# Performance work log

Measured on AMD Instinct MI355X. Metric: run time of the kernel, lower is better.

The kernel has to match this reference:

```python
import jax, jax.numpy as jnp
import numpy as np

T, H, N = 4096, 2048, 1024  # seq_length, d_model, d_hidden
MAX_PHASE = 6.28


def setup_inputs() -> dict:
    key = jax.random.key(0)
    ks = jax.random.split(key, 9)
    inputs = jax.random.normal(ks[0], (T, H), dtype=jnp.float32)
    # LRU init (exp_param=True, r_min=0, r_max=1): lambda = exp(-exp(nu) + i*exp(theta))
    u1 = jax.random.uniform(ks[1], (N,), dtype=jnp.float32)
    u2 = jax.random.uniform(ks[2], (N,), dtype=jnp.float32)
    nu = jnp.log(-0.5 * jnp.log(u1))            # log-parameterized decay
    theta = jnp.log(MAX_PHASE * u2)             # log-parameterized phase
    # gamma_log = log(sqrt(1 - |lambda|^2)), |lambda| = exp(-exp(nu))
    gamma_log = 0.5 * jnp.log(1.0 - jnp.exp(-2.0 * jnp.exp(nu)) + 1e-8)
    B_re = jax.random.normal(ks[3], (N, H), dtype=jnp.float32) / np.sqrt(2 * H)
    B_im = jax.random.normal(ks[4], (N, H), dtype=jnp.float32) / np.sqrt(2 * H)
    C_re = jax.random.normal(ks[5], (H, N), dtype=jnp.float32) / np.sqrt(N)
    C_im = jax.random.normal(ks[6], (H, N), dtype=jnp.float32) / np.sqrt(N)
    D = jax.random.normal(ks[7], (H,), dtype=jnp.float32)
    return {"inputs": inputs, "nu": nu, "theta": theta, "gamma_log": gamma_log,
            "B_re": B_re, "B_im": B_im, "C_re": C_re, "C_im": C_im, "D": D}


def _binary_operator_diag(q_i, q_j):
    A_i, b_i = q_i
    A_j, b_j = q_j
    return (A_j * A_i, A_j * b_i + b_j)


def reference(inputs, nu, theta, gamma_log, B_re, B_im, C_re, C_im, D):
    # diag_lambda = exp(-exp(nu) + i*exp(theta))   (exp_param=True)
    diag_lambda = jnp.exp(-jnp.exp(nu) + 1j * jnp.exp(theta))      # [N] complex64
    gamma = jnp.exp(gamma_log)                                      # [N]
    B_norm = (B_re + 1j * B_im) * gamma[:, None]                    # [N, H] complex
    # Bu_t = B_norm @ u_t  ->  [T, N]
    Bu = inputs.astype(jnp.complex64) @ B_norm.T
    Lam = jnp.broadcast_to(diag_lambda[None, :], Bu.shape)          # [T, N]
    # parallel scan of diagonal linear recurrence h_t = lambda * h_{t-1} + Bu_t
    _, h = jax.lax.associative_scan(_binary_operator_diag, (Lam, Bu))
    C = C_re + 1j * C_im                                            # [H, N]
    # y_t = Re(C @ h_t) + D * u_t
    y = (h @ C.T).real + D[None, :] * inputs                        # [T, H]
    return y
```

## Files before the change

### kernel.cpp

```cpp
#include <hip/hip_runtime.h>
#include <math.h>

#define T_DIM 4096
#define H_DIM 2048
#define N_DIM 1024
#define N2    2048
#define KK    2048
#define CHUNK 64
#define NCHUNK (T_DIM / CHUNK)
#define NT    (KK / 64)

using u16    = unsigned short;
using u16x4  = __attribute__((ext_vector_type(4))) u16;
using bf16x8 = __attribute__((ext_vector_type(8))) short;
using f32x4  = __attribute__((ext_vector_type(4))) float;

typedef const __attribute__((address_space(1))) u16 glob_u16;
typedef __attribute__((address_space(3))) u16 lds_u16;

__device__ inline void gload16(const u16* g, u16* l) {
    __builtin_amdgcn_global_load_lds((glob_u16*)g, (lds_u16*)l, 16, 0, 0);
}

__device__ inline u16 f2bf(float x) {
    unsigned u = __builtin_bit_cast(unsigned, x);
    u += 0x7fffu + ((u >> 16) & 1u);
    return (u16)(u >> 16);
}
__device__ inline float bf2f(u16 x) {
    return __builtin_bit_cast(float, (unsigned)x << 16);
}

__global__ __launch_bounds__(256) void cvt_u_k(const float* __restrict__ X,
                                               u16* __restrict__ Y) {
    size_t i = ((size_t)blockIdx.x * 256 + threadIdx.x) * 4;
    float4 v = *(const float4*)(X + i);
    u16x4 o = { f2bf(v.x), f2bf(v.y), f2bf(v.z), f2bf(v.w) };
    *(u16x4*)(Y + i) = o;
}

__global__ __launch_bounds__(256) void cvt_b_k(const float* __restrict__ Bre,
                                               const float* __restrict__ Bim,
                                               const float* __restrict__ glog,
                                               u16* __restrict__ Bcat) {
    size_t i = ((size_t)blockIdx.x * 256 + threadIdx.x) * 4;
    int n = (int)(i >> 11);
    size_t h = i & 2047;
    int nn = n & (N_DIM - 1);
    float g = expf(glog[nn]);
    const float* src = (n < N_DIM ? Bre : Bim) + (size_t)nn * H_DIM + h;
    float4 v = *(const float4*)src;
    u16x4 o = { f2bf(v.x * g), f2bf(v.y * g), f2bf(v.z * g), f2bf(v.w * g) };
    *(u16x4*)(Bcat + i) = o;
}

__global__ __launch_bounds__(256) void cvt_c_k(const float* __restrict__ Cre,
                                               const float* __restrict__ Cim,
                                               u16* __restrict__ Ccat) {
    size_t i = ((size_t)blockIdx.x * 256 + threadIdx.x) * 4;
    int hrow = (int)(i >> 11);
    int n = (int)(i & 2047);
    float sgn = 1.f;
    const float* src;
    if (n < N_DIM) src = Cre + (size_t)hrow * N_DIM + n;
    else { src = Cim + (size_t)hrow * N_DIM + (n - N_DIM); sgn = -1.f; }
    float4 v = *(const float4*)src;
    u16x4 o = { f2bf(v.x * sgn), f2bf(v.y * sgn), f2bf(v.z * sgn), f2bf(v.w * sgn) };
    *(u16x4*)(Ccat + i) = o;
}

template <int EPI>
__global__ __launch_bounds__(512, 2) void gemm_pipe(
    const u16* __restrict__ A, const u16* __restrict__ B,
    float* __restrict__ C, const float* __restrict__ D,
    const u16* __restrict__ Ubf)
{
    __shared__ u16 lds[65536];

    const int tid  = threadIdx.x;
    const int wave = tid >> 6, lane = tid & 63;
    const int nbid = (blockIdx.x & 7) * 32 + (blockIdx.x >> 3);
    const int bm = nbid >> 4;
    const int bn = nbid & 15;
    const size_t row0 = (size_t)bm * 256;
    const size_t col0 = (size_t)bn * 128;
    const int wr = wave >> 1, wc = wave & 1;
    const int fr = lane & 15, fq = lane >> 4;

    const int srow = tid >> 3;
    const int skc  = (tid & 7) ^ (srow & 7);
    const u16* aSrc = A + (row0 + srow) * KK + skc * 8;
    const u16* bSrc = B + (col0 + srow) * KK + skc * 8;

    const int aBase = (wr * 64 + fr) * 64;
    const int bBase = (wc * 64 + fr) * 64;
    const int swzk[2] = { ((fq) ^ (fr & 7)) * 8, ((4 + fq) ^ (fr & 7)) * 8 };

    f32x4 acc[4][4] = {};

    auto STAGE_A = [&](int buf, int kt) {
#pragma unroll
        for (int u = 0; u < 4; ++u)
            gload16(aSrc + (size_t)u * 64 * KK + kt * 64,
                    &lds[buf * 16384 + u * 4096 + wave * 512]);
    };
    auto STAGE_B = [&](int buf, int kt) {
#pragma unroll
        for (int u = 0; u < 2; ++u)
            gload16(bSrc + (size_t)u * 64 * KK + kt * 64,
                    &lds[49152 + buf * 8192 + u * 4096 + wave * 512]);
    };

    STAGE_A(0, 0); STAGE_B(0, 0); STAGE_A(1, 1);
    asm volatile("s_waitcnt vmcnt(4)\n\ts_barrier" ::: "memory");

    int a_cur = 0;
#pragma unroll 2
    for (int t = 0; t < NT; ++t) {
        const u16* Ab = &lds[a_cur * 16384];
        const u16* Bb = &lds[49152 + (t & 1) * 8192];
        bf16x8 af[4], bfv[4];

#pragma unroll
        for (int m = 0; m < 4; ++m)
            af[m] = *(const bf16x8*)&Ab[aBase + m * 1024 + swzk[0]];
#pragma unroll
        for (int n = 0; n < 4; ++n)
            bfv[n] = *(const bf16x8*)&Bb[bBase + n * 1024 + swzk[0]];
        if (t + 1 < NT) STAGE_B((t + 1) & 1, t + 1);
        asm volatile("s_barrier\n\ts_waitcnt lgkmcnt(0)" ::: "memory");
        __builtin_amdgcn_s_setprio(1);
#pragma unroll
        for (int m = 0; m < 4; ++m)
#pragma unroll
            for (int n = 0; n < 4; ++n)
                acc[m][n] = __builtin_amdgcn_mfma_f32_16x16x32_bf16(
                    af[m], bfv[n], acc[m][n], 0, 0, 0);
        __builtin_amdgcn_s_setprio(0);
        asm volatile("s_barrier" ::: "memory");

#pragma unroll
        for (int m = 0; m < 4; ++m)
            af[m] = *(const bf16x8*)&Ab[aBase + m * 1024 + swzk[1]];
#pragma unroll
        for (int n = 0; n < 4; ++n)
            bfv[n] = *(const bf16x8*)&Bb[bBase + n * 1024 + swzk[1]];
        if (t + 2 < NT) {
            int a_nxt = a_cur - 1; if (a_nxt < 0) a_nxt = 2;
            STAGE_A(a_nxt, t + 2);
        }
        if (t + 2 < NT)
            asm volatile("s_waitcnt vmcnt(4)\n\ts_barrier\n\ts_waitcnt lgkmcnt(0)" ::: "memory");
        else if (t + 1 < NT)
            asm volatile("s_waitcnt vmcnt(0)\n\ts_barrier\n\ts_waitcnt lgkmcnt(0)" ::: "memory");
        else
            asm volatile("s_barrier\n\ts_waitcnt lgkmcnt(0)" ::: "memory");
        __builtin_amdgcn_s_setprio(1);
#pragma unroll
        for (int m = 0; m < 4; ++m)
#pragma unroll
            for (int n = 0; n < 4; ++n)
                acc[m][n] = __builtin_amdgcn_mfma_f32_16x16x32_bf16(
                    af[m], bfv[n], acc[m][n], 0, 0, 0);
        __builtin_amdgcn_s_setprio(0);
        asm volatile("s_barrier" ::: "memory");

        ++a_cur; if (a_cur == 3) a_cur = 0;
    }

    const int crow = (int)row0 + wr * 64 + fq * 4;
    const int ccol = (int)col0 + wc * 64 + fr;
    float dc[4];
    if constexpr (EPI) {
#pragma unroll
        for (int n = 0; n < 4; ++n) dc[n] = D[ccol + n * 16];
    }
#pragma unroll
    for (int m = 0; m < 4; ++m)
#pragma unroll
        for (int n = 0; n < 4; ++n) {
            int cc = ccol + n * 16;
#pragma unroll
            for (int j = 0; j < 4; ++j) {
                int r = crow + m * 16 + j;
                size_t p = (size_t)r * N2 + cc;
                float v = acc[m][n][j];
                if constexpr (EPI) v += dc[n] * bf2f(Ubf[p]);
                C[p] = v;
            }
        }
}

__global__ __launch_bounds__(256) void carry_pass_k(const float* __restrict__ Bu,
                                                    const float* __restrict__ nu,
                                                    const float* __restrict__ theta,
                                                    float* __restrict__ car) {
    int idx = blockIdx.x * 256 + threadIdx.x;
    int chan = idx & (N_DIM - 1);
    int chunk = idx >> 10;
    float a = expf(nu[chan]), b = expf(theta[chan]);
    float m = expf(-a), s, c;
    __sincosf(b, &s, &c);
    float lr = m * c, li = m * s;
    float hr = 0.f, hi = 0.f;
    size_t base = (size_t)chunk * CHUNK * N2 + chan;
    for (int i = 0; i < CHUNK; ++i) {
        size_t p = base + (size_t)i * N2;
        float br = Bu[p], bi = Bu[p + N_DIM];
        float nr = fmaf(lr, hr, fmaf(-li, hi, br));
        float ni = fmaf(lr, hi, fmaf(li, hr, bi));
        hr = nr; hi = ni;
    }
    car[(size_t)chunk * N2 + chan] = hr;
    car[(size_t)chunk * N2 + N_DIM + chan] = hi;
}

__global__ __launch_bounds__(256) void scan_carry_k(float* __restrict__ car,
                                                    const float* __restrict__ nu,
                                                    const float* __restrict__ theta) {
    __shared__ float sR[NCHUNK][65], sI[NCHUNK][65];
    int tid = threadIdx.x;
    int chan0 = blockIdx.x * 64;
    for (int i = tid; i < NCHUNK * 64; i += 256) {
        int ck = i >> 6, c = i & 63;
        sR[ck][c] = car[(size_t)ck * N2 + chan0 + c];
        sI[ck][c] = car[(size_t)ck * N2 + N_DIM + chan0 + c];
    }
    __syncthreads();
    if (tid < 64) {
        int chan = chan0 + tid;
        float a = expf(nu[chan]), b = expf(theta[chan]);
        float m = expf(-(float)CHUNK * a), s, c;
        __sincosf((float)CHUNK * b, &s, &c);
        float lr = m * c, li = m * s;
        float hr = sR[0][tid], hi = sI[0][tid];
        for (int ck = 1; ck < NCHUNK; ++ck) {
            float nr = fmaf(lr, hr, fmaf(-li, hi, sR[ck][tid]));
            float ni = fmaf(lr, hi, fmaf(li, hr, sI[ck][tid]));
            hr = nr; hi = ni;
            sR[ck][tid] = hr; sI[ck][tid] = hi;
        }
    }
    __syncthreads();
    for (int i = tid; i < NCHUNK * 64; i += 256) {
        int ck = i >> 6, c = i & 63;
        car[(size_t)ck * N2 + chan0 + c] = sR[ck][c];
        car[(size_t)ck * N2 + N_DIM + chan0 + c] = sI[ck][c];
    }
}

__global__ __launch_bounds__(256) void scan_out_k(const float* __restrict__ Bu,
                                                  const float* __restrict__ car,
                                                  const float* __restrict__ nu,
                                                  const float* __restrict__ theta,
                                                  u16* __restrict__ Hbf) {
    int idx = blockIdx.x * 256 + threadIdx.x;
    int chan = idx & (N_DIM - 1);
    int chunk = idx >> 10;
    float a = expf(nu[chan]), b = expf(theta[chan]);
    float m = expf(-a), s, c;
    __sincosf(b, &s, &c);
    float lr = m * c, li = m * s;
    float hr = 0.f, hi = 0.f;
    if (chunk > 0) {
        size_t cp = (size_t)(chunk - 1) * N2 + chan;
        hr = car[cp]; hi = car[cp + N_DIM];
    }
    size_t base = (size_t)chunk * CHUNK * N2 + chan;
    for (int i = 0; i < CHUNK; ++i) {
        size_t p = base + (size_t)i * N2;
        float br = Bu[p], bi = Bu[p + N_DIM];
        float nr = fmaf(lr, hr, fmaf(-li, hi, br));
        float ni = fmaf(lr, hi, fmaf(li, hr, bi));
        hr = nr; hi = ni;
        Hbf[p] = f2bf(hr);
        Hbf[p + N_DIM] = f2bf(hi);
    }
}

extern "C" void kernel_launch(void* const* d_in, const int* in_sizes, int n_in,
                              void* d_out, int out_size, void* d_ws, size_t ws_size,
                              hipStream_t stream) {
    const float* U     = (const float*)d_in[0];
    const float* nu    = (const float*)d_in[1];
    const float* theta = (const float*)d_in[2];
    const float* glog  = (const float*)d_in[3];
    const float* Bre   = (const float*)d_in[4];
    const float* Bim   = (const float*)d_in[5];
    const float* Cre   = (const float*)d_in[6];
    const float* Cim   = (const float*)d_in[7];
    const float* Dp    = (const float*)d_in[8];
    float* Y = (float*)d_out;

    u16* Ubf  = (u16*)d_ws;
    u16* Bcat = Ubf + (size_t)T_DIM * H_DIM;
    u16* Ccat = Bcat + (size_t)N2 * H_DIM;
    u16* Hbf  = Ccat + (size_t)H_DIM * N2;
    float* Bu = (float*)(Hbf + (size_t)T_DIM * N2);
    float* car = Bu + (size_t)T_DIM * N2;

    cvt_u_k<<<(T_DIM * H_DIM / 4) / 256, 256, 0, stream>>>(U, Ubf);
    cvt_b_k<<<((size_t)N2 * H_DIM / 4) / 256, 256, 0, stream>>>(Bre, Bim, glog, Bcat);
    cvt_c_k<<<((size_t)H_DIM * N2 / 4) / 256, 256, 0, stream>>>(Cre, Cim, Ccat);

    gemm_pipe<0><<<256, 512, 0, stream>>>(Ubf, Bcat, Bu, nullptr, nullptr);

    carry_pass_k<<<(NCHUNK * N_DIM) / 256, 256, 0, stream>>>(Bu, nu, theta, car);
    scan_carry_k<<<N_DIM / 64, 256, 0, stream>>>(car, nu, theta);
    scan_out_k<<<(NCHUNK * N_DIM) / 256, 256, 0, stream>>>(Bu, car, nu, theta, Hbf);

    gemm_pipe<1><<<256, 512, 0, stream>>>(Hbf, Ccat, Y, Dp, Ubf);
}
```

Baseline: 121.7 us.

## Software-pipeline LDS fragment reads across iterations and cut per-iteration barriers

The GEMM main loop now keeps two sets of register fragments. The first-half fragments of the next K tile are read from LDS right after a single barrier at the end of each iteration, while the second-half reads sit between the two MFMA groups. This drops the loop from four barriers per iteration to one and lets LDS reads overlap MFMA work. Launch bounds move from 2 to 1 blocks per CU, giving the compiler room for the extra fragment registers. The risk is higher register pressure and less latency hiding from the compiler's own scheduling, since the unroll pragma was also removed.

```diff
diff --git a/kernel.cpp b/kernel.cpp
--- a/kernel.cpp
+++ b/kernel.cpp
@@ -70,7 +70,7 @@
 }
 
 template <int EPI>
-__global__ __launch_bounds__(512, 2) void gemm_pipe(
+__global__ __launch_bounds__(512, 1) void gemm_pipe(
     const u16* __restrict__ A, const u16* __restrict__ B,
     float* __restrict__ C, const float* __restrict__ D,
     const u16* __restrict__ Ubf)
@@ -94,7 +94,8 @@
 
     const int aBase = (wr * 64 + fr) * 64;
     const int bBase = (wc * 64 + fr) * 64;
-    const int swzk[2] = { ((fq) ^ (fr & 7)) * 8, ((4 + fq) ^ (fr & 7)) * 8 };
+    const int swz0 = ((fq)     ^ (fr & 7)) * 8;
+    const int swz1 = ((4 + fq) ^ (fr & 7)) * 8;
 
     f32x4 acc[4][4] = {};
 
@@ -111,60 +112,67 @@
                     &lds[49152 + buf * 8192 + u * 4096 + wave * 512]);
     };
 
+    bf16x8 fa[4], fb[4], ga[4], gb[4];
+
+    auto READ_F = [&](const u16* Ab, const u16* Bb, int swz) {
+#pragma unroll
+        for (int m = 0; m < 4; ++m) fa[m] = *(const bf16x8*)&Ab[aBase + m * 1024 + swz];
+#pragma unroll
+        for (int n = 0; n < 4; ++n) fb[n] = *(const bf16x8*)&Bb[bBase + n * 1024 + swz];
+    };
+    auto READ_G = [&](const u16* Ab, const u16* Bb, int swz) {
+#pragma unroll
+        for (int m = 0; m < 4; ++m) ga[m] = *(const bf16x8*)&Ab[aBase + m * 1024 + swz];
+#pragma unroll
+        for (int n = 0; n < 4; ++n) gb[n] = *(const bf16x8*)&Bb[bBase + n * 1024 + swz];
+    };
+    auto MFMA_F = [&]() {
+        __builtin_amdgcn_s_setprio(1);
+#pragma unroll
+        for (int m = 0; m < 4; ++m)
+#pragma unroll
+            for (int n = 0; n < 4; ++n)
+                acc[m][n] = __builtin_amdgcn_mfma_f32_16x16x32_bf16(
+                    fa[m], fb[n], acc[m][n], 0, 0, 0);
+        __builtin_amdgcn_s_setprio(0);
+    };
+    auto MFMA_G = [&]() {
+        __builtin_amdgcn_s_setprio(1);
+#pragma unroll
+        for (int m = 0; m < 4; ++m)
+#pragma unroll
+            for (int n = 0; n < 4; ++n)
+                acc[m][n] = __builtin_amdgcn_mfma_f32_16x16x32_bf16(
+                    ga[m], gb[n], acc[m][n], 0, 0, 0);
+        __builtin_amdgcn_s_setprio(0);
+    };
+
     STAGE_A(0, 0); STAGE_B(0, 0); STAGE_A(1, 1);
-    asm volatile("s_waitcnt vmcnt(4)\n\ts_barrier" ::: "memory");
+    asm volatile("s_waitcnt vmcnt(4)" ::: "memory");
+    __builtin_amdgcn_s_barrier();
+    READ_F(&lds[0], &lds[49152], swz0);
 
     int a_cur = 0;
-#pragma unroll 2
     for (int t = 0; t < NT; ++t) {
         const u16* Ab = &lds[a_cur * 16384];
         const u16* Bb = &lds[49152 + (t & 1) * 8192];
-        bf16x8 af[4], bfv[4];
-
-#pragma unroll
-        for (int m = 0; m < 4; ++m)
-            af[m] = *(const bf16x8*)&Ab[aBase + m * 1024 + swzk[0]];
-#pragma unroll
-        for (int n = 0; n < 4; ++n)
-            bfv[n] = *(const bf16x8*)&Bb[bBase + n * 1024 + swzk[0]];
+
         if (t + 1 < NT) STAGE_B((t + 1) & 1, t + 1);
-        asm volatile("s_barrier\n\ts_waitcnt lgkmcnt(0)" ::: "memory");
-        __builtin_amdgcn_s_setprio(1);
-#pragma unroll
-        for (int m = 0; m < 4; ++m)
-#pragma unroll
-            for (int n = 0; n < 4; ++n)
-                acc[m][n] = __builtin_amdgcn_mfma_f32_16x16x32_bf16(
-                    af[m], bfv[n], acc[m][n], 0, 0, 0);
-        __builtin_amdgcn_s_setprio(0);
-        asm volatile("s_barrier" ::: "memory");
-
-#pragma unroll
-        for (int m = 0; m < 4; ++m)
-            af[m] = *(const bf16x8*)&Ab[aBase + m * 1024 + swzk[1]];
-#pragma unroll
-        for (int n = 0; n < 4; ++n)
-            bfv[n] = *(const bf16x8*)&Bb[bBase + n * 1024 + swzk[1]];
+        MFMA_F();
         if (t + 2 < NT) {
             int a_nxt = a_cur - 1; if (a_nxt < 0) a_nxt = 2;
             STAGE_A(a_nxt, t + 2);
         }
-        if (t + 2 < NT)
-            asm volatile("s_waitcnt vmcnt(4)\n\ts_barrier\n\ts_waitcnt lgkmcnt(0)" ::: "memory");
-        else if (t + 1 < NT)
-            asm volatile("s_waitcnt vmcnt(0)\n\ts_barrier\n\ts_waitcnt lgkmcnt(0)" ::: "memory");
-        else
-            asm volatile("s_barrier\n\ts_waitcnt lgkmcnt(0)" ::: "memory");
-        __builtin_amdgcn_s_setprio(1);
-#pragma unroll
-        for (int m = 0; m < 4; ++m)
-#pragma unroll
-            for (int n = 0; n < 4; ++n)
-                acc[m][n] = __builtin_amdgcn_mfma_f32_16x16x32_bf16(
-                    af[m], bfv[n], acc[m][n], 0, 0, 0);
-        __builtin_amdgcn_s_setprio(0);
-        asm volatile("s_barrier" ::: "memory");
-
+        READ_G(Ab, Bb, swz1);
+        MFMA_G();
+
+        if (t + 1 < NT) {
+            if (t + 2 < NT) asm volatile("s_waitcnt vmcnt(4)" ::: "memory");
+            else            asm volatile("s_waitcnt vmcnt(0)" ::: "memory");
+            __builtin_amdgcn_s_barrier();
+            int a_n = a_cur + 1; if (a_n == 3) a_n = 0;
+            READ_F(&lds[a_n * 16384], &lds[49152 + ((t + 1) & 1) * 8192], swz0);
+        }
         ++a_cur; if (a_cur == 3) a_cur = 0;
     }
 
```

New measurement: 114.9 us. 5.6% less time.
